# Performance work log

Measured on AMD Instinct MI355X. Metric: run time of the kernel, lower is better.

## Reference

```python
import jax, jax.numpy as jnp
import numpy as np

N_NODES = 100000
N_EDGES = 600000
D_IN = 128
D_OUT = 96
N_REL = 4


def setup_inputs() -> dict:
    key = jax.random.key(0)
    ks = jax.random.split(key, 9)
    s = 1.0 / np.sqrt(D_IN)
    return {
        "classic_features": jax.random.normal(ks[0], (N_NODES, D_IN), jnp.float32),
        "edge_index": jax.random.randint(ks[1], (2, N_EDGES), 0, N_NODES),
        "edge_type": jax.random.randint(ks[2], (N_EDGES,), 0, N_REL),
        "W1": jax.random.uniform(ks[3], (N_REL, D_IN, D_IN), jnp.float32, -s, s),
        "root1": jax.random.uniform(ks[4], (D_IN, D_IN), jnp.float32, -s, s),
        "b1": jnp.zeros((D_IN,), jnp.float32),
        "W2": jax.random.uniform(ks[5], (N_REL, D_IN, D_OUT), jnp.float32, -s, s),
        "root2": jax.random.uniform(ks[6], (D_IN, D_OUT), jnp.float32, -s, s),
        "b2": jnp.zeros((D_OUT,), jnp.float32),
    }


def _rgcn_layer(x, src, dst, etype, W, root, b):
    # x: [N, d_in]; W: [R, d_in, d_out]
    n = x.shape[0]
    r = W.shape[0]
    # relation-specific transform of all nodes: [R, N, d_out]
    H = jnp.einsum('nd,rde->rne', x, W)
    msgs = H[etype, src]  # [E, d_out] gather per-edge transformed source feature
    # per-relation in-degree for mean aggregation (PyG RGCNConv mean norm)
    cnt = jnp.zeros((n, r), x.dtype).at[dst, etype].add(1.0)
    norm = 1.0 / jnp.maximum(cnt[dst, etype], 1.0)  # [E]
    agg = jnp.zeros((n, W.shape[-1]), x.dtype).at[dst].add(norm[:, None] * msgs)
    return agg + x @ root + b


def reference(classic_features, edge_index, edge_type, W1, root1, b1, W2, root2, b2):
    src, dst = edge_index[0], edge_index[1]
    h = _rgcn_layer(classic_features, src, dst, edge_type, W1, root1, b1)
    h = jax.nn.relu(h)  # dropout is identity in eval mode
    out = _rgcn_layer(h, src, dst, edge_type, W2, root2, b2)
    return out
```

## Files before the change

### kernel.cpp

```cpp
#include <hip/hip_runtime.h>

#define NN 100000
#define NE 600000
#define D  128
#define DOUT2 96
#define NREL 4
#define KREL 512
#define KCAT 640
#define SCAN_B 98

typedef short short8 __attribute__((ext_vector_type(8)));
typedef float f32x4  __attribute__((ext_vector_type(4)));

__device__ __forceinline__ ushort f2bf(float x) {
    unsigned u = __builtin_bit_cast(unsigned, x);
    u += 0x7fffu + ((u >> 16) & 1u);
    return (ushort)(u >> 16);
}
__device__ __forceinline__ float bfhi(unsigned u) {
    return __builtin_bit_cast(float, u & 0xffff0000u);
}
__device__ __forceinline__ float bflo(unsigned u) {
    return __builtin_bit_cast(float, u << 16);
}

__global__ void prep0(const float* __restrict__ x, ushort* __restrict__ Xb,
                      const float* __restrict__ W1, const float* __restrict__ root1,
                      short* __restrict__ Wp1,
                      const float* __restrict__ W2, const float* __restrict__ root2,
                      short* __restrict__ Wp2,
                      float* __restrict__ cnt, int* __restrict__ fill) {
    int i = blockIdx.x * 256 + threadIdx.x;
    const int S0 = (NN * NREL) / 4;
    const int S1 = NN / 4;
    const int S2 = (NN * D) / 4;
    const int S3 = KCAT * D;
    const int S4 = KCAT * DOUT2;
    if (i < S0) { ((float4*)cnt)[i] = make_float4(0.f, 0.f, 0.f, 0.f); return; }
    i -= S0;
    if (i < S1) { ((int4*)fill)[i] = make_int4(0, 0, 0, 0); return; }
    i -= S1;
    if (i < S2) {
        float4 v = ((const float4*)x)[i];
        ushort4 o;
        o.x = f2bf(v.x); o.y = f2bf(v.y); o.z = f2bf(v.z); o.w = f2bf(v.w);
        ((ushort4*)Xb)[i] = o;
        return;
    }
    i -= S2;
    if (i < S3) {
        int j = i & 7, rest = i >> 3;
        int n = rest % D, kq = rest / D;
        int k = kq * 8 + j;
        float v = (k < KREL) ? W1[(size_t)k * D + n] : root1[(size_t)(k - KREL) * D + n];
        Wp1[i] = (short)f2bf(v);
        return;
    }
    i -= S3;
    if (i < S4) {
        int j = i & 7, rest = i >> 3;
        int n = rest % DOUT2, kq = rest / DOUT2;
        int k = kq * 8 + j;
        float v = (k < KREL) ? W2[(size_t)k * DOUT2 + n] : root2[(size_t)(k - KREL) * DOUT2 + n];
        Wp2[i] = (short)f2bf(v);
        return;
    }
}

__global__ void count_deg(const int* __restrict__ dst,
                          const int* __restrict__ et,
                          float* __restrict__ cnt) {
    int e = blockIdx.x * blockDim.x + threadIdx.x;
    if (e < NE) unsafeAtomicAdd(&cnt[dst[e] * NREL + et[e]], 1.0f);
}

__global__ void scan1(const float* __restrict__ cnt, int* __restrict__ bsum) {
    __shared__ int s[256];
    int tid = threadIdx.x;
    int base = blockIdx.x * 1024 + tid * 4;
    int t = 0;
    for (int i = 0; i < 4; i++) {
        int v = base + i;
        if (v < NN) {
            float4 c = *(const float4*)&cnt[(size_t)v * 4];
            t += (int)(c.x + c.y + c.z + c.w);
        }
    }
    s[tid] = t; __syncthreads();
    for (int o = 128; o > 0; o >>= 1) {
        if (tid < o) s[tid] += s[tid + o];
        __syncthreads();
    }
    if (tid == 0) bsum[blockIdx.x] = s[0];
}

__global__ void scan2(int* __restrict__ bsum) {
    __shared__ int s[128];
    int tid = threadIdx.x;
    int mine = (tid < SCAN_B) ? bsum[tid] : 0;
    s[tid] = mine; __syncthreads();
    for (int o = 1; o < 128; o <<= 1) {
        int v = (tid >= o) ? s[tid - o] : 0;
        __syncthreads();
        s[tid] += v;
        __syncthreads();
    }
    if (tid < SCAN_B) bsum[tid] = s[tid] - mine;
}

__global__ void scan3(const float* __restrict__ cnt, const int* __restrict__ bsum,
                      int* __restrict__ off) {
    __shared__ int s[256];
    int tid = threadIdx.x;
    int base = blockIdx.x * 1024 + tid * 4;
    int d[4]; int t = 0;
    for (int i = 0; i < 4; i++) {
        int v = base + i; d[i] = 0;
        if (v < NN) {
            float4 c = *(const float4*)&cnt[(size_t)v * 4];
            d[i] = (int)(c.x + c.y + c.z + c.w);
        }
        t += d[i];
    }
    int mine = t;
    s[tid] = t; __syncthreads();
    for (int o = 1; o < 256; o <<= 1) {
        int v = (tid >= o) ? s[tid - o] : 0;
        __syncthreads();
        s[tid] += v;
        __syncthreads();
    }
    int ex = s[tid] - mine + bsum[blockIdx.x];
    for (int i = 0; i < 4; i++) {
        int v = base + i;
        if (v < NN) { off[v] = ex; ex += d[i]; }
    }
    if (blockIdx.x == 0 && tid == 0) off[NN] = NE;
}

__global__ void bucket_edges(const int* __restrict__ src, const int* __restrict__ dst,
                             const int* __restrict__ et, const int* __restrict__ off,
                             int* __restrict__ fill, int* __restrict__ srcpk) {
    int e = blockIdx.x * blockDim.x + threadIdx.x;
    if (e >= NE) return;
    int dn = dst[e];
    int pos = off[dn] + atomicAdd(&fill[dn], 1);
    srcpk[pos] = (src[e] << 2) | et[e];
}

template <int BN, bool RELU, bool OUT_BF16>
__global__ __launch_bounds__(256, 5) void rgcn_fused(
    const ushort* __restrict__ Xb,
    const int*   __restrict__ srcpk,
    const int*   __restrict__ off,
    const float* __restrict__ cnt,
    const short* __restrict__ Wcp,
    const float* __restrict__ bias,
    void*        __restrict__ Cout,
    int M) {
    constexpr int NFW = (BN / 16 + 1) / 2;
    __shared__ short At[64 * 32 * 8];

    const int tid  = threadIdx.x;
    const int wave = tid >> 6;
    const int lane = tid & 63;
    const int l    = lane & 15;
    const int qw   = lane >> 4;
    const int g    = wave * 4 + qw;
    const int v0   = blockIdx.x * 32;

#pragma unroll
    for (int half = 0; half < 2; half++) {
        int nv = g + half * 16;
        int v  = v0 + nv;
        float acc[4][8];
#pragma unroll
        for (int r = 0; r < 4; r++)
#pragma unroll
            for (int j = 0; j < 8; j++) acc[r][j] = 0.0f;

        float4 c4 = *(const float4*)&cnt[(size_t)v * 4];
        float nrm0 = 1.0f / fmaxf(c4.x, 1.0f);
        float nrm1 = 1.0f / fmaxf(c4.y, 1.0f);
        float nrm2 = 1.0f / fmaxf(c4.z, 1.0f);
        float nrm3 = 1.0f / fmaxf(c4.w, 1.0f);
        int e = off[v], end = off[v + 1];

#define EDGE_ACC(PK, XB) {                                                  \
        int t_ = (PK) & 3;                                                  \
        float s0 = (t_ == 0) ? nrm0 : 0.0f;                                 \
        float s1 = (t_ == 1) ? nrm1 : 0.0f;                                 \
        float s2 = (t_ == 2) ? nrm2 : 0.0f;                                 \
        float s3 = (t_ == 3) ? nrm3 : 0.0f;                                 \
        float xf[8];                                                        \
        xf[0] = bflo(XB.x); xf[1] = bfhi(XB.x);                             \
        xf[2] = bflo(XB.y); xf[3] = bfhi(XB.y);                             \
        xf[4] = bflo(XB.z); xf[5] = bfhi(XB.z);                             \
        xf[6] = bflo(XB.w); xf[7] = bfhi(XB.w);                             \
        _Pragma("unroll")                                                   \
        for (int j = 0; j < 8; j++) {                                       \
            acc[0][j] += s0 * xf[j];                                        \
            acc[1][j] += s1 * xf[j];                                        \
            acc[2][j] += s2 * xf[j];                                        \
            acc[3][j] += s3 * xf[j];                                        \
        } }

        for (; e + 3 < end; e += 4) {
            int p0 = srcpk[e],     p1 = srcpk[e + 1];
            int p2 = srcpk[e + 2], p3 = srcpk[e + 3];
            uint4 x0 = *(const uint4*)&Xb[(size_t)(p0 >> 2) * D + l * 8];
            uint4 x1 = *(const uint4*)&Xb[(size_t)(p1 >> 2) * D + l * 8];
            uint4 x2 = *(const uint4*)&Xb[(size_t)(p2 >> 2) * D + l * 8];
            uint4 x3 = *(const uint4*)&Xb[(size_t)(p3 >> 2) * D + l * 8];
            EDGE_ACC(p0, x0); EDGE_ACC(p1, x1);
            EDGE_ACC(p2, x2); EDGE_ACC(p3, x3);
        }
        for (; e < end; e++) {
            int p0 = srcpk[e];
            uint4 x0 = *(const uint4*)&Xb[(size_t)(p0 >> 2) * D + l * 8];
            EDGE_ACC(p0, x0);
        }
#undef EDGE_ACC

#pragma unroll
        for (int r = 0; r < 4; r++) {
            short8 w;
#pragma unroll
            for (int j = 0; j < 8; j++) w[j] = (short)f2bf(acc[r][j]);
            int kq = r * 16 + l;
            *(short8*)&At[(kq * 32 + (nv ^ (kq & 7))) * 8] = w;
        }
    }

    const int m16   = l;
    const int q     = qw;
    const int mt    = wave & 1;
    const int nbase = (wave >> 1) * NFW * 16;
    f32x4 acc2[NFW];
#pragma unroll
    for (int i = 0; i < NFW; i++) acc2[i] = (f32x4)0.0f;

    {
        int rowc = v0 + mt * 16 + m16;
        const ushort* Xrow = Xb + (size_t)rowc * D;
#pragma unroll
        for (int s2 = 0; s2 < 4; s2++) {
            short8 af = *(const short8*)&Xrow[s2 * 32 + q * 8];
            const short* bbase = Wcp + ((size_t)((16 + s2) * 4 + q) * BN + nbase + m16) * 8;
#pragma unroll
            for (int nf = 0; nf < NFW; nf++) {
                short8 bf = *(const short8*)(bbase + nf * 128);
                acc2[nf] = __builtin_amdgcn_mfma_f32_16x16x32_bf16(af, bf, acc2[nf], 0, 0, 0);
            }
        }
    }

    __syncthreads();

#pragma unroll 4
    for (int ks = 0; ks < 16; ks++) {
        int kq = ks * 4 + q;
        short8 af = *(const short8*)&At[(kq * 32 + ((mt * 16 + m16) ^ (kq & 7))) * 8];
        const short* bbase = Wcp + ((size_t)kq * BN + nbase + m16) * 8;
#pragma unroll
        for (int nf = 0; nf < NFW; nf++) {
            short8 bf = *(const short8*)(bbase + nf * 128);
            acc2[nf] = __builtin_amdgcn_mfma_f32_16x16x32_bf16(af, bf, acc2[nf], 0, 0, 0);
        }
    }

#pragma unroll
    for (int nf = 0; nf < NFW; nf++) {
        int n = nbase + nf * 16 + m16;
        float b = bias[n];
#pragma unroll
        for (int r = 0; r < 4; r++) {
            int m = v0 + mt * 16 + q * 4 + r;
            float vv = acc2[nf][r] + b;
            if (RELU) vv = fmaxf(vv, 0.0f);
            if (OUT_BF16) ((ushort*)Cout)[(size_t)m * BN + n] = f2bf(vv);
            else          ((float*)Cout)[(size_t)m * BN + n]  = vv;
        }
    }
}

extern "C" void kernel_launch(void* const* d_in, const int* in_sizes, int n_in,
                              void* d_out, int out_size, void* d_ws, size_t ws_size,
                              hipStream_t stream) {
    const float* x     = (const float*)d_in[0];
    const int*   ei    = (const int*)d_in[1];
    const int*   et    = (const int*)d_in[2];
    const float* W1    = (const float*)d_in[3];
    const float* root1 = (const float*)d_in[4];
    const float* b1    = (const float*)d_in[5];
    const float* W2    = (const float*)d_in[6];
    const float* root2 = (const float*)d_in[7];
    const float* b2    = (const float*)d_in[8];
    const int* srcp = ei;
    const int* dstp = ei + NE;
    float* out = (float*)d_out;

    short*  Wp1  = (short*)d_ws;
    short*  Wp2  = Wp1 + (size_t)KCAT * D;
    ushort* Xb   = (ushort*)(Wp2 + (size_t)KCAT * DOUT2);
    ushort* h    = Xb + (size_t)NN * D;
    float*  cnt  = (float*)(h + (size_t)NN * D);
    int*    off  = (int*)(cnt + (size_t)NN * NREL);
    int*    fill = off + (NN + 1);
    int*    bsum = fill + NN;
    int*    srcpk= bsum + 128;

    {
        const int S = (NN * NREL) / 4 + NN / 4 + (NN * D) / 4 + KCAT * D + KCAT * DOUT2;
        prep0<<<(S + 255) / 256, 256, 0, stream>>>(x, Xb, W1, root1, Wp1,
                                                   W2, root2, Wp2, cnt, fill);
    }
    count_deg<<<(NE + 255) / 256, 256, 0, stream>>>(dstp, et, cnt);
    scan1<<<SCAN_B, 256, 0, stream>>>(cnt, bsum);
    scan2<<<1, 128, 0, stream>>>(bsum);
    scan3<<<SCAN_B, 256, 0, stream>>>(cnt, bsum, off);
    bucket_edges<<<(NE + 255) / 256, 256, 0, stream>>>(srcp, dstp, et, off, fill, srcpk);

    const int fblocks = NN / 32;

    rgcn_fused<128, true, true><<<fblocks, 256, 0, stream>>>(
        Xb, srcpk, off, cnt, Wp1, b1, h, NN);
    rgcn_fused<96, false, false><<<fblocks, 256, 0, stream>>>(
        h, srcpk, off, cnt, Wp2, b2, out, NN);
}
```

Before: 324.6 us.

## Shrink fused RGCN tile to 16 nodes per block and raise occupancy

New measurement: 461.8 us. 42.3% more time.

```diff
diff --git a/kernel.cpp b/kernel.cpp
--- a/kernel.cpp
+++ b/kernel.cpp
@@ -149,7 +149,7 @@
 }
 
 template <int BN, bool RELU, bool OUT_BF16>
-__global__ __launch_bounds__(256, 5) void rgcn_fused(
+__global__ __launch_bounds__(256, 8) void rgcn_fused(
     const ushort* __restrict__ Xb,
     const int*   __restrict__ srcpk,
     const int*   __restrict__ off,
@@ -158,8 +158,7 @@
     const float* __restrict__ bias,
     void*        __restrict__ Cout,
     int M) {
-    constexpr int NFW = (BN / 16 + 1) / 2;
-    __shared__ short At[64 * 32 * 8];
+    __shared__ short At[64 * 16 * 8];
 
     const int tid  = threadIdx.x;
     const int wave = tid >> 6;
@@ -167,12 +166,10 @@
     const int l    = lane & 15;
     const int qw   = lane >> 4;
     const int g    = wave * 4 + qw;
-    const int v0   = blockIdx.x * 32;
-
-#pragma unroll
-    for (int half = 0; half < 2; half++) {
-        int nv = g + half * 16;
-        int v  = v0 + nv;
+    const int v0   = blockIdx.x * 16;
+
+    {
+        int v = v0 + g;
         float acc[4][8];
 #pragma unroll
         for (int r = 0; r < 4; r++)
@@ -228,30 +225,29 @@
 #pragma unroll
             for (int j = 0; j < 8; j++) w[j] = (short)f2bf(acc[r][j]);
             int kq = r * 16 + l;
-            *(short8*)&At[(kq * 32 + (nv ^ (kq & 7))) * 8] = w;
-        }
-    }
-
-    const int m16   = l;
-    const int q     = qw;
-    const int mt    = wave & 1;
-    const int nbase = (wave >> 1) * NFW * 16;
-    f32x4 acc2[NFW];
-#pragma unroll
-    for (int i = 0; i < NFW; i++) acc2[i] = (f32x4)0.0f;
+            *(short8*)&At[(kq * 16 + (g ^ (kq & 7))) * 8] = w;
+        }
+    }
+
+    const int m16  = l;
+    const int q    = qw;
+    const int nb0  = wave * 16;
+    const int nb1  = 64 + wave * 16;
+    const bool has1 = (nb1 < BN);
+    f32x4 a0 = (f32x4)0.0f, a1 = (f32x4)0.0f;
 
     {
-        int rowc = v0 + mt * 16 + m16;
+        int rowc = v0 + m16;
         const ushort* Xrow = Xb + (size_t)rowc * D;
 #pragma unroll
         for (int s2 = 0; s2 < 4; s2++) {
             short8 af = *(const short8*)&Xrow[s2 * 32 + q * 8];
-            const short* bbase = Wcp + ((size_t)((16 + s2) * 4 + q) * BN + nbase + m16) * 8;
-#pragma unroll
-            for (int nf = 0; nf < NFW; nf++) {
-                short8 bf = *(const short8*)(bbase + nf * 128);
-                acc2[nf] = __builtin_amdgcn_mfma_f32_16x16x32_bf16(af, bf, acc2[nf], 0, 0, 0);
-            }
+            size_t kqb = (size_t)((16 + s2) * 4 + q) * BN;
+            a0 = __builtin_amdgcn_mfma_f32_16x16x32_bf16(
+                af, *(const short8*)(Wcp + (kqb + nb0 + m16) * 8), a0, 0, 0, 0);
+            if (has1)
+                a1 = __builtin_amdgcn_mfma_f32_16x16x32_bf16(
+                    af, *(const short8*)(Wcp + (kqb + nb1 + m16) * 8), a1, 0, 0, 0);
         }
     }
 
@@ -260,23 +256,34 @@
 #pragma unroll 4
     for (int ks = 0; ks < 16; ks++) {
         int kq = ks * 4 + q;
-        short8 af = *(const short8*)&At[(kq * 32 + ((mt * 16 + m16) ^ (kq & 7))) * 8];
-        const short* bbase = Wcp + ((size_t)kq * BN + nbase + m16) * 8;
-#pragma unroll
-        for (int nf = 0; nf < NFW; nf++) {
-            short8 bf = *(const short8*)(bbase + nf * 128);
-            acc2[nf] = __builtin_amdgcn_mfma_f32_16x16x32_bf16(af, bf, acc2[nf], 0, 0, 0);
-        }
-    }
-
-#pragma unroll
-    for (int nf = 0; nf < NFW; nf++) {
-        int n = nbase + nf * 16 + m16;
+        short8 af = *(const short8*)&At[(kq * 16 + (m16 ^ (kq & 7))) * 8];
+        size_t kqb = (size_t)kq * BN;
+        a0 = __builtin_amdgcn_mfma_f32_16x16x32_bf16(
+            af, *(const short8*)(Wcp + (kqb + nb0 + m16) * 8), a0, 0, 0, 0);
+        if (has1)
+            a1 = __builtin_amdgcn_mfma_f32_16x16x32_bf16(
+                af, *(const short8*)(Wcp + (kqb + nb1 + m16) * 8), a1, 0, 0, 0);
+    }
+
+    {
+        int n = nb0 + m16;
         float b = bias[n];
 #pragma unroll
         for (int r = 0; r < 4; r++) {
-            int m = v0 + mt * 16 + q * 4 + r;
-            float vv = acc2[nf][r] + b;
+            int m = v0 + q * 4 + r;
+            float vv = a0[r] + b;
+            if (RELU) vv = fmaxf(vv, 0.0f);
+            if (OUT_BF16) ((ushort*)Cout)[(size_t)m * BN + n] = f2bf(vv);
+            else          ((float*)Cout)[(size_t)m * BN + n]  = vv;
+        }
+    }
+    if (has1) {
+        int n = nb1 + m16;
+        float b = bias[n];
+#pragma unroll
+        for (int r = 0; r < 4; r++) {
+            int m = v0 + q * 4 + r;
+            float vv = a1[r] + b;
             if (RELU) vv = fmaxf(vv, 0.0f);
             if (OUT_BF16) ((ushort*)Cout)[(size_t)m * BN + n] = f2bf(vv);
             else          ((float*)Cout)[(size_t)m * BN + n]  = vv;
@@ -321,7 +328,7 @@
     scan3<<<SCAN_B, 256, 0, stream>>>(cnt, bsum, off);
     bucket_edges<<<(NE + 255) / 256, 256, 0, stream>>>(srcp, dstp, et, off, fill, srcpk);
 
-    const int fblocks = NN / 32;
+    const int fblocks = NN / 16;
 
     rgcn_fused<128, true, true><<<fblocks, 256, 0, stream>>>(
         Xb, srcpk, off, cnt, Wp1, b1, h, NN);
```

## Sort edges by relation within each destination bucket to drop per-edge masking

Applied to the files above, without the earlier changes.

New measurement: 366.8 us. +13.0%, slower.

```diff
diff --git a/kernel.cpp b/kernel.cpp
--- a/kernel.cpp
+++ b/kernel.cpp
@@ -32,7 +32,7 @@
                       float* __restrict__ cnt, int* __restrict__ fill) {
     int i = blockIdx.x * 256 + threadIdx.x;
     const int S0 = (NN * NREL) / 4;
-    const int S1 = NN / 4;
+    const int S1 = NN;
     const int S2 = (NN * D) / 4;
     const int S3 = KCAT * D;
     const int S4 = KCAT * DOUT2;
@@ -140,12 +140,19 @@
 
 __global__ void bucket_edges(const int* __restrict__ src, const int* __restrict__ dst,
                              const int* __restrict__ et, const int* __restrict__ off,
-                             int* __restrict__ fill, int* __restrict__ srcpk) {
+                             int* __restrict__ fill, int* __restrict__ srcpk,
+                             const float* __restrict__ cnt) {
     int e = blockIdx.x * blockDim.x + threadIdx.x;
     if (e >= NE) return;
     int dn = dst[e];
-    int pos = off[dn] + atomicAdd(&fill[dn], 1);
-    srcpk[pos] = (src[e] << 2) | et[e];
+    int t  = et[e];
+    float4 c4 = *(const float4*)&cnt[(size_t)dn * 4];
+    int base = off[dn];
+    if (t > 0) base += (int)c4.x;
+    if (t > 1) base += (int)c4.y;
+    if (t > 2) base += (int)c4.z;
+    int pos = base + atomicAdd(&fill[dn * 4 + t], 1);
+    srcpk[pos] = src[e];
 }
 
 template <int BN, bool RELU, bool OUT_BF16>
@@ -173,63 +180,48 @@
     for (int half = 0; half < 2; half++) {
         int nv = g + half * 16;
         int v  = v0 + nv;
-        float acc[4][8];
-#pragma unroll
-        for (int r = 0; r < 4; r++)
-#pragma unroll
-            for (int j = 0; j < 8; j++) acc[r][j] = 0.0f;
 
         float4 c4 = *(const float4*)&cnt[(size_t)v * 4];
-        float nrm0 = 1.0f / fmaxf(c4.x, 1.0f);
-        float nrm1 = 1.0f / fmaxf(c4.y, 1.0f);
-        float nrm2 = 1.0f / fmaxf(c4.z, 1.0f);
-        float nrm3 = 1.0f / fmaxf(c4.w, 1.0f);
-        int e = off[v], end = off[v + 1];
-
-#define EDGE_ACC(PK, XB) {                                                  \
-        int t_ = (PK) & 3;                                                  \
-        float s0 = (t_ == 0) ? nrm0 : 0.0f;                                 \
-        float s1 = (t_ == 1) ? nrm1 : 0.0f;                                 \
-        float s2 = (t_ == 2) ? nrm2 : 0.0f;                                 \
-        float s3 = (t_ == 3) ? nrm3 : 0.0f;                                 \
-        float xf[8];                                                        \
-        xf[0] = bflo(XB.x); xf[1] = bfhi(XB.x);                             \
-        xf[2] = bflo(XB.y); xf[3] = bfhi(XB.y);                             \
-        xf[4] = bflo(XB.z); xf[5] = bfhi(XB.z);                             \
-        xf[6] = bflo(XB.w); xf[7] = bfhi(XB.w);                             \
-        _Pragma("unroll")                                                   \
-        for (int j = 0; j < 8; j++) {                                       \
-            acc[0][j] += s0 * xf[j];                                        \
-            acc[1][j] += s1 * xf[j];                                        \
-            acc[2][j] += s2 * xf[j];                                        \
-            acc[3][j] += s3 * xf[j];                                        \
-        } }
-
-        for (; e + 3 < end; e += 4) {
-            int p0 = srcpk[e],     p1 = srcpk[e + 1];
-            int p2 = srcpk[e + 2], p3 = srcpk[e + 3];
-            uint4 x0 = *(const uint4*)&Xb[(size_t)(p0 >> 2) * D + l * 8];
-            uint4 x1 = *(const uint4*)&Xb[(size_t)(p1 >> 2) * D + l * 8];
-            uint4 x2 = *(const uint4*)&Xb[(size_t)(p2 >> 2) * D + l * 8];
-            uint4 x3 = *(const uint4*)&Xb[(size_t)(p3 >> 2) * D + l * 8];
-            EDGE_ACC(p0, x0); EDGE_ACC(p1, x1);
-            EDGE_ACC(p2, x2); EDGE_ACC(p3, x3);
-        }
-        for (; e < end; e++) {
-            int p0 = srcpk[e];
-            uint4 x0 = *(const uint4*)&Xb[(size_t)(p0 >> 2) * D + l * 8];
-            EDGE_ACC(p0, x0);
-        }
-#undef EDGE_ACC
+        int e = off[v];
+
+#define ACC8(XB) {                                                          \
+        acc[0] += bflo(XB.x); acc[1] += bfhi(XB.x);                         \
+        acc[2] += bflo(XB.y); acc[3] += bfhi(XB.y);                         \
+        acc[4] += bflo(XB.z); acc[5] += bfhi(XB.z);                         \
+        acc[6] += bflo(XB.w); acc[7] += bfhi(XB.w); }
 
 #pragma unroll
         for (int r = 0; r < 4; r++) {
+            float cf = (r == 0) ? c4.x : (r == 1) ? c4.y : (r == 2) ? c4.z : c4.w;
+            int cr  = (int)cf;
+            int end = e + cr;
+            float acc[8];
+#pragma unroll
+            for (int j = 0; j < 8; j++) acc[j] = 0.0f;
+
+            for (; e + 3 < end; e += 4) {
+                int p0 = srcpk[e],     p1 = srcpk[e + 1];
+                int p2 = srcpk[e + 2], p3 = srcpk[e + 3];
+                uint4 x0 = *(const uint4*)&Xb[(size_t)p0 * D + l * 8];
+                uint4 x1 = *(const uint4*)&Xb[(size_t)p1 * D + l * 8];
+                uint4 x2 = *(const uint4*)&Xb[(size_t)p2 * D + l * 8];
+                uint4 x3 = *(const uint4*)&Xb[(size_t)p3 * D + l * 8];
+                ACC8(x0); ACC8(x1); ACC8(x2); ACC8(x3);
+            }
+            for (; e < end; e++) {
+                int p0 = srcpk[e];
+                uint4 x0 = *(const uint4*)&Xb[(size_t)p0 * D + l * 8];
+                ACC8(x0);
+            }
+
+            float nrm = 1.0f / fmaxf(cf, 1.0f);
             short8 w;
 #pragma unroll
-            for (int j = 0; j < 8; j++) w[j] = (short)f2bf(acc[r][j]);
+            for (int j = 0; j < 8; j++) w[j] = (short)f2bf(acc[j] * nrm);
             int kq = r * 16 + l;
             *(short8*)&At[(kq * 32 + (nv ^ (kq & 7))) * 8] = w;
         }
+#undef ACC8
     }
 
     const int m16   = l;
@@ -307,11 +299,11 @@
     float*  cnt  = (float*)(h + (size_t)NN * D);
     int*    off  = (int*)(cnt + (size_t)NN * NREL);
     int*    fill = off + (NN + 1);
-    int*    bsum = fill + NN;
+    int*    bsum = fill + (size_t)NN * 4;
     int*    srcpk= bsum + 128;
 
     {
-        const int S = (NN * NREL) / 4 + NN / 4 + (NN * D) / 4 + KCAT * D + KCAT * DOUT2;
+        const int S = (NN * NREL) / 4 + NN + (NN * D) / 4 + KCAT * D + KCAT * DOUT2;
         prep0<<<(S + 255) / 256, 256, 0, stream>>>(x, Xb, W1, root1, Wp1,
                                                    W2, root2, Wp2, cnt, fill);
     }
@@ -319,7 +311,8 @@
     scan1<<<SCAN_B, 256, 0, stream>>>(cnt, bsum);
     scan2<<<1, 128, 0, stream>>>(bsum);
     scan3<<<SCAN_B, 256, 0, stream>>>(cnt, bsum, off);
-    bucket_edges<<<(NE + 255) / 256, 256, 0, stream>>>(srcp, dstp, et, off, fill, srcpk);
+    bucket_edges<<<(NE + 255) / 256, 256, 0, stream>>>(srcp, dstp, et, off, fill,
+                                                       srcpk, cnt);
 
     const int fblocks = NN / 32;
 
```
